# Optimization experiments

Measured on AMD Instinct MI355X. Metric: run time of the kernel, lower is better.

The kernel has to match this reference:

```python
import jax, jax.numpy as jnp
import numpy as np

B, T, C, H = 2, 2048, 1024, 16
D = C // H  # head dim = 64


def setup_inputs() -> dict:
    key = jax.random.key(0)
    ks = jax.random.split(key, 3)
    x = jax.random.normal(ks[0], (B, T, C), dtype=jnp.float32)
    W_attn = jax.random.normal(ks[1], (C, 3 * C), dtype=jnp.float32) * (1.0 / np.sqrt(C))
    b_attn = jnp.zeros((3 * C,), dtype=jnp.float32)
    W_proj = jax.random.normal(ks[2], (C, C), dtype=jnp.float32) * (1.0 / np.sqrt(C))
    b_proj = jnp.zeros((C,), dtype=jnp.float32)
    return {"x": x, "W_attn": W_attn, "b_attn": b_attn, "W_proj": W_proj, "b_proj": b_proj}


def reference(x, W_attn, b_attn, W_proj, b_proj):
    Bb, Tt, Cc = x.shape
    qkv = x @ W_attn + b_attn                       # [B,T,3C]
    q, k, v = jnp.split(qkv, 3, axis=-1)            # each [B,T,C]
    q = q.reshape(Bb, Tt, H, D).transpose(0, 2, 1, 3)  # [B,H,T,D]
    k = k.reshape(Bb, Tt, H, D).transpose(0, 2, 1, 3)
    v = v.reshape(Bb, Tt, H, D).transpose(0, 2, 1, 3)
    # NOTE: original scales by 1/sqrt(n_embd), not 1/sqrt(head_dim)
    scale = 1.0 / np.sqrt(Cc)
    wei = jnp.einsum('bhqd,bhkd->bhqk', q, k) * scale  # [B,H,T,T]
    causal = jnp.tril(jnp.ones((Tt, Tt), dtype=bool))
    wei = jnp.where(causal, wei, -jnp.inf)
    wei = jax.nn.softmax(wei, axis=-1)
    out = jnp.einsum('bhqk,bhkd->bhqd', wei, v)        # [B,H,T,D]
    out = out.transpose(0, 2, 1, 3).reshape(Bb, Tt, Cc)
    return out @ W_proj + b_proj
```

## Files before the change

kernel.cpp:

```cpp
#include <hip/hip_runtime.h>


typedef short bfrag __attribute__((ext_vector_type(8)));
typedef float facc  __attribute__((ext_vector_type(4)));
typedef float f16v  __attribute__((ext_vector_type(16)));
typedef float f4v   __attribute__((ext_vector_type(4)));
typedef unsigned int u32x2 __attribute__((ext_vector_type(2)));
typedef unsigned int u32x4v __attribute__((ext_vector_type(4)));
typedef unsigned short u16;

#define MFMA16(a, b, c) __builtin_amdgcn_mfma_f32_16x16x32_bf16((a), (b), (c), 0, 0, 0)
#define MFMA32(a, b, c) __builtin_amdgcn_mfma_f32_32x32x16_bf16((a), (b), (c), 0, 0, 0)

__device__ __forceinline__ u16 f2bf(float f) {
  union { float f; unsigned u; } v; v.f = f;
  unsigned r = v.u + 0x7fffu + ((v.u >> 16) & 1u);
  return (u16)(r >> 16);
}

__device__ __forceinline__ unsigned cvtpk(float lo, float hi) {
  unsigned r;
  asm("v_cvt_pk_bf16_f32 %0, %1, %2" : "=v"(r) : "v"(lo), "v"(hi));
  return r;
}

__device__ __forceinline__ void async_lds16(const void* g, void* l) {
  __builtin_amdgcn_global_load_lds(
      (const __attribute__((address_space(1))) unsigned char*)g,
      (__attribute__((address_space(3))) unsigned char*)l, 16, 0, 0);
}


__global__ void cast_bf16_kernel(const float* __restrict__ s, u16* __restrict__ d, int n) {
  int i = (blockIdx.x * blockDim.x + threadIdx.x) * 4;
  if (i >= n) return;
  f4v v = *reinterpret_cast<const f4v*>(s + i);
  u32x2 w;
  w[0] = (unsigned)f2bf(v[0]) | ((unsigned)f2bf(v[1]) << 16);
  w[1] = (unsigned)f2bf(v[2]) | ((unsigned)f2bf(v[3]) << 16);
  *reinterpret_cast<u32x2*>(d + i) = w;
}

__global__ void transpose_cast_kernel(const float* __restrict__ src, u16* __restrict__ dst,
                                      int K, int N) {
  __shared__ float tile[32][33];
  int tx = threadIdx.x, ty = threadIdx.y;
  int n0 = blockIdx.x * 32, k0 = blockIdx.y * 32;
  for (int j = ty; j < 32; j += 8)
    tile[j][tx] = src[(size_t)(k0 + j) * N + (n0 + tx)];
  __syncthreads();
  for (int j = ty; j < 32; j += 8)
    dst[(size_t)(n0 + j) * K + (k0 + tx)] = f2bf(tile[tx][j]);
}


template <int EPI>
__global__ __launch_bounds__(256) void gemm_kernel(
    const u16* __restrict__ A, const u16* __restrict__ Bt,
    const float* __restrict__ bias, float* __restrict__ outf,
    u16* __restrict__ qb, u16* __restrict__ kb, u16* __restrict__ vb, int NX) {
  constexpr int KD = 1024, NK = KD / 32;
  __shared__ u16 As[2][128 * 32];
  __shared__ u16 Bs[2][128 * 32];
  const int t = threadIdx.x;
  const int l = t & 63, w = t >> 6;
  const int wm = w >> 1, wn = w & 1;
  const int lg = l >> 4, lc = l & 15;
  const int nwg = gridDim.x;
  const int u = blockIdx.x;
  const int swz = (u & 7) * (nwg >> 3) + (u >> 3);
  const int m0 = (swz / NX) * 128, n0 = (swz % NX) * 128;
  facc acc[4][4] = {};
  const int srow = t >> 2, scol = (t & 3) * 8;
  const u16* ga = A + (size_t)(m0 + srow) * KD + scol;
  const u16* gb = Bt + (size_t)(n0 + srow) * KD + scol;

#define GSTAGE(bi, kt_)                                                          \
  {                                                                              \
    async_lds16(ga + (kt_) * 32, As[bi] + t * 8);                                \
    async_lds16(ga + 64 * KD + (kt_) * 32, As[bi] + 2048 + t * 8);               \
    async_lds16(gb + (kt_) * 32, Bs[bi] + t * 8);                                \
    async_lds16(gb + 64 * KD + (kt_) * 32, Bs[bi] + 2048 + t * 8);               \
  }

  GSTAGE(0, 0);
  __syncthreads();
  for (int kt = 0; kt < NK; ++kt) {
    const int buf = kt & 1;
    if (kt + 1 < NK) GSTAGE(buf ^ 1, kt + 1);
    bfrag a[4], b[4];
#pragma unroll
    for (int mi = 0; mi < 4; ++mi)
      a[mi] = *reinterpret_cast<const bfrag*>(As[buf] + (wm * 64 + mi * 16 + lc) * 32 + lg * 8);
#pragma unroll
    for (int ni = 0; ni < 4; ++ni)
      b[ni] = *reinterpret_cast<const bfrag*>(Bs[buf] + (wn * 64 + ni * 16 + lc) * 32 + lg * 8);
#pragma unroll
    for (int mi = 0; mi < 4; ++mi)
#pragma unroll
      for (int ni = 0; ni < 4; ++ni)
        acc[mi][ni] = MFMA16(a[mi], b[ni], acc[mi][ni]);
    __syncthreads();
  }
#undef GSTAGE
#pragma unroll
  for (int mi = 0; mi < 4; ++mi) {
#pragma unroll
    for (int ni = 0; ni < 4; ++ni) {
#pragma unroll
      for (int r = 0; r < 4; ++r) {
        int gm = m0 + wm * 64 + mi * 16 + lg * 4 + r;
        int gn = n0 + wn * 64 + ni * 16 + lc;
        float val = acc[mi][ni][r] + bias[gn];
        if constexpr (EPI == 0) {
          int sec = gn >> 10, ci = gn & 1023;
          int h = ci >> 6, d = ci & 63;
          int b_ = gm >> 11, tq = gm & 2047;
          int bh = b_ * 16 + h;
          if (sec == 0) {
            qb[((size_t)bh * 2048 + tq) * 64 + d] = f2bf(val * 0.045084439f);
          } else if (sec == 1) {
            kb[((size_t)bh * 2048 + tq) * 64 + d] = f2bf(val);
          } else {
            vb[((size_t)bh * 64 + d) * 2048 + tq] = f2bf(val);
          }
        } else {
          outf[(size_t)gm * 1024 + gn] = val;
        }
      }
    }
  }
}


__global__ __launch_bounds__(256, 2) void attn_kernel(
    const u16* __restrict__ Qb, const u16* __restrict__ Kb,
    const u16* __restrict__ Vtb, u16* __restrict__ attn) {
  constexpr int T = 2048;
  __shared__ u16 Ks[2][2][64 * 64];
  const int t = threadIdx.x;
  const int l = t & 63, w = t >> 6;
  const int wq = w >> 1, ws = w & 1;
  const int c = l & 31, h = l >> 5;
  const int b = blockIdx.x;
  const int bh = b & 31;
  const int qblk = 31 - (b >> 5);
  const int ntile = qblk + 1;
  const int nrounds = (ntile + 1) >> 1;
  const int q0 = qblk * 64 + wq * 32;
  const size_t base = (size_t)bh * T * 64;
  const u16* Qp = Qb + base;
  const u16* Kp = Kb + base;
  const u16* Vp = Vtb + base;

  bfrag qf[4];
#pragma unroll
  for (int dt = 0; dt < 4; ++dt)
    qf[dt] = *reinterpret_cast<const bfrag*>(Qp + (size_t)(q0 + c) * 64 + dt * 16 + 8 * h);

  f16v o[2] = {};
  f16v s[2];
  float m_ = -1e30f, l_ = 0.f;

  const int srow0 = wq * 8 + (l >> 3);
  const int sw8   = ((l & 7) ^ ((l >> 3) & 7)) * 8;
  const int ldso  = wq * 512 + l * 8;

#define STAGE_K(p, tile_)                                                        \
  {                                                                              \
    _Pragma("unroll")                                                            \
    for (int j = 0; j < 4; ++j)                                                  \
      async_lds16(Kp + (size_t)(64 * (tile_) + srow0 + 16 * j) * 64 + sw8,       \
                  &Ks[p][ws][ldso + 1024 * j]);                                  \
  }
#define LOADV(vf, kvb_)                                                          \
  {                                                                              \
    _Pragma("unroll")                                                            \
    for (int nt = 0; nt < 2; ++nt)                                               \
      _Pragma("unroll")                                                          \
      for (int k2 = 0; k2 < 4; ++k2)                                             \
        vf[nt * 4 + k2] = *reinterpret_cast<const bfrag*>(                       \
            Vp + (size_t)(32 * nt + c) * T + (kvb_) + 16 * k2 + 8 * h);          \
  }

  auto qk = [&](const u16* ks) {
    const f16v z = {};
    s[0] = z; s[1] = z;
    __builtin_amdgcn_s_setprio(1);
#pragma unroll
    for (int kt = 0; kt < 2; ++kt)
#pragma unroll
      for (int dt = 0; dt < 4; ++dt) {
        const bfrag a = *reinterpret_cast<const bfrag*>(
            ks + (32 * kt + c) * 64 + (((2 * dt + h) ^ (c & 7)) * 8));
        s[kt] = MFMA32(a, qf[dt], s[kt]);
      }
    __builtin_amdgcn_s_setprio(0);
  };

  auto pv = [&](const bfrag pa[4], const bfrag vf[8]) {
    __builtin_amdgcn_s_setprio(1);
#pragma unroll
    for (int nt = 0; nt < 2; ++nt)
#pragma unroll
      for (int k2 = 0; k2 < 4; ++k2)
        o[nt] = MFMA32(pa[k2], vf[nt * 4 + k2], o[nt]);
    __builtin_amdgcn_s_setprio(0);
  };

  auto softmax_pa = [&](int it, bfrag pa[4]) {
    if (it == ntile - 1) {
      const int kvb = 64 * it;
      const int qq = q0 + c;
#pragma unroll
      for (int kt = 0; kt < 2; ++kt)
#pragma unroll
        for (int r = 0; r < 16; ++r) {
          const int kk = kvb + 32 * kt + (r & 3) + 8 * (r >> 2) + 4 * h;
          if (kk > qq) s[kt][r] = -1e30f;
        }
    }
    float pms[4] = {-1e30f, -1e30f, -1e30f, -1e30f};
#pragma unroll
    for (int kt = 0; kt < 2; ++kt)
#pragma unroll
      for (int r = 0; r < 16; ++r) pms[r & 3] = fmaxf(pms[r & 3], s[kt][r]);
    float pm = fmaxf(fmaxf(pms[0], pms[1]), fmaxf(pms[2], pms[3]));
    pm = fmaxf(pm, __shfl_xor(pm, 32));
    if (!__all(pm <= m_ + 8.0f)) {
      const float mn = fmaxf(m_, pm);
      const float al = exp2f(m_ - mn);
      l_ *= al;
#pragma unroll
      for (int r = 0; r < 16; ++r) {
        const float ar = __shfl(al, (r & 3) + 8 * (r >> 2) + 4 * h);
        o[0][r] *= ar;
        o[1][r] *= ar;
      }
      m_ = mn;
    }
    float ps[4] = {0.f, 0.f, 0.f, 0.f};
#pragma unroll
    for (int kt = 0; kt < 2; ++kt)
#pragma unroll
      for (int r = 0; r < 16; ++r) {
        const float e = exp2f(s[kt][r] - m_);
        s[kt][r] = e;
        ps[r & 3] += e;
      }
    float pss = (ps[0] + ps[1]) + (ps[2] + ps[3]);
    pss += __shfl_xor(pss, 32);
    l_ += pss;
#pragma unroll
    for (int kt = 0; kt < 2; ++kt)
#pragma unroll
      for (int sub = 0; sub < 2; ++sub) {
        const int bs = 8 * sub;
        unsigned x1 = cvtpk(s[kt][bs + 0], s[kt][bs + 1]);
        unsigned y1 = cvtpk(s[kt][bs + 4], s[kt][bs + 5]);
        asm volatile("v_permlane32_swap_b32 %0, %1" : "+v"(x1), "+v"(y1));
        unsigned x2 = cvtpk(s[kt][bs + 2], s[kt][bs + 3]);
        unsigned y2 = cvtpk(s[kt][bs + 6], s[kt][bs + 7]);
        asm volatile("v_permlane32_swap_b32 %0, %1" : "+v"(x2), "+v"(y2));
        union { u32x4v wv; bfrag f; } u;
        u.wv[0] = x1; u.wv[1] = x2; u.wv[2] = y1; u.wv[3] = y2;
        pa[2 * kt + sub] = u.f;
      }
  };

  bfrag vfA[8], vfB[8], pa[4];
  if (ws < ntile) { STAGE_K(0, ws); LOADV(vfA, 64 * ws); }
  __syncthreads();
  for (int r = 0; r < nrounds; ++r) {
    const int p = r & 1;
    const int it = 2 * r + ws;
    const int itn = it + 2;
    if (itn < ntile) {
      STAGE_K(p ^ 1, itn);
      if (p) { LOADV(vfA, 64 * itn); } else { LOADV(vfB, 64 * itn); }
    }
    if (it < ntile) {
      qk(&Ks[p][ws][0]);
      softmax_pa(it, pa);
      pv(pa, p ? vfB : vfA);
    }
    __syncthreads();
  }

  float* Fo = (float*)&Ks[0][0][0];
  float* Fm = Fo + 2 * 64 * 33;
  float* Fl = Fm + 64;
  if (ws == 1) {
#pragma unroll
    for (int nt = 0; nt < 2; ++nt)
#pragma unroll
      for (int r = 0; r < 16; ++r) {
        const int row = (r & 3) + 8 * (r >> 2) + 4 * h;
        Fo[(wq * 64 + nt * 32 + c) * 33 + row] = o[nt][r];
      }
    if (h == 0) { Fm[wq * 32 + c] = m_; Fl[wq * 32 + c] = l_; }
  }
  __syncthreads();
  if (ws == 0) {
    const float m1v = Fm[wq * 32 + c], l1v = Fl[wq * 32 + c];
    const float mm = fmaxf(m_, m1v);
    const float a0 = exp2f(m_ - mm), a1 = exp2f(m1v - mm);
    const float linv = 1.0f / (a0 * l_ + a1 * l1v);
    const int b_ = bh >> 4, hd = bh & 15;
#pragma unroll
    for (int r = 0; r < 16; ++r) {
      const int row = (r & 3) + 8 * (r >> 2) + 4 * h;
      const float a0r = __shfl(a0, row);
      const float a1r = __shfl(a1, row);
      const float lr = __shfl(linv, row);
      const int tq = q0 + row;
#pragma unroll
      for (int nt = 0; nt < 2; ++nt) {
        const float o1 = Fo[(wq * 64 + nt * 32 + c) * 33 + row];
        attn[((size_t)(b_ * T + tq)) * 1024 + hd * 64 + 32 * nt + c] =
            f2bf((a0r * o[nt][r] + a1r * o1) * lr);
      }
    }
  }
#undef STAGE_K
#undef LOADV
}


extern "C" void kernel_launch(void* const* d_in, const int* in_sizes, int n_in,
                              void* d_out, int out_size, void* d_ws, size_t ws_size,
                              hipStream_t stream) {
  const float* x      = (const float*)d_in[0];
  const float* W_attn = (const float*)d_in[1];
  const float* b_attn = (const float*)d_in[2];
  const float* W_proj = (const float*)d_in[3];
  const float* b_proj = (const float*)d_in[4];
  float* out = (float*)d_out;
  char* ws = (char*)d_ws;
  u16* xb   = (u16*)(ws);
  u16* Wat  = (u16*)(ws + (8u  << 20));
  u16* Wpt  = (u16*)(ws + (14u << 20));
  u16* Qb   = (u16*)(ws + (16u << 20));
  u16* Kb   = (u16*)(ws + (24u << 20));
  u16* Vtb  = (u16*)(ws + (32u << 20));
  u16* attn = (u16*)(ws + (40u << 20));

  cast_bf16_kernel<<<4096, 256, 0, stream>>>(x, xb, 4096 * 1024);
  transpose_cast_kernel<<<dim3(96, 32), dim3(32, 8), 0, stream>>>(W_attn, Wat, 1024, 3072);
  transpose_cast_kernel<<<dim3(32, 32), dim3(32, 8), 0, stream>>>(W_proj, Wpt, 1024, 1024);
  gemm_kernel<0><<<768, 256, 0, stream>>>(xb, Wat, b_attn, nullptr, Qb, Kb, Vtb, 24);
  attn_kernel<<<1024, 256, 0, stream>>>(Qb, Kb, Vtb, attn);
  gemm_kernel<1><<<256, 256, 0, stream>>>(attn, Wpt, b_proj, out, nullptr, nullptr, nullptr, 8);
}
```

Measured before the change: 148.7 us.

## Drop GEMM double buffering and XCD swizzle, reorder attention query blocks

The GEMM goes back to a single LDS buffer, loading each K-slice between two barriers so the global-to-LDS copy no longer overlaps with MFMA work. It also drops the XCD-aware block swizzle in favour of a plain 2D grid. Separately, the attention kernel's query-block order changes from strictly longest-first to an interleaved long/short sequence across groups of 8, aiming at better load balance. The GEMM changes remove overlap and L2 locality, and the new attention order may leave long blocks in the tail.

After: 151.9 us. 2.2% more time.

```diff
diff --git a/kernel.cpp b/kernel.cpp
--- a/kernel.cpp
+++ b/kernel.cpp
@@ -58,51 +58,41 @@
 __global__ __launch_bounds__(256) void gemm_kernel(
     const u16* __restrict__ A, const u16* __restrict__ Bt,
     const float* __restrict__ bias, float* __restrict__ outf,
-    u16* __restrict__ qb, u16* __restrict__ kb, u16* __restrict__ vb, int NX) {
-  constexpr int KD = 1024, NK = KD / 32;
-  __shared__ u16 As[2][128 * 32];
-  __shared__ u16 Bs[2][128 * 32];
+    u16* __restrict__ qb, u16* __restrict__ kb, u16* __restrict__ vb) {
+  constexpr int KD = 1024;
+  __shared__ u16 As[128 * 32];
+  __shared__ u16 Bs[128 * 32];
   const int t = threadIdx.x;
   const int l = t & 63, w = t >> 6;
   const int wm = w >> 1, wn = w & 1;
   const int lg = l >> 4, lc = l & 15;
-  const int nwg = gridDim.x;
-  const int u = blockIdx.x;
-  const int swz = (u & 7) * (nwg >> 3) + (u >> 3);
-  const int m0 = (swz / NX) * 128, n0 = (swz % NX) * 128;
+  const int m0 = blockIdx.y * 128, n0 = blockIdx.x * 128;
   facc acc[4][4] = {};
   const int srow = t >> 2, scol = (t & 3) * 8;
   const u16* ga = A + (size_t)(m0 + srow) * KD + scol;
   const u16* gb = Bt + (size_t)(n0 + srow) * KD + scol;
-
-#define GSTAGE(bi, kt_)                                                          \
-  {                                                                              \
-    async_lds16(ga + (kt_) * 32, As[bi] + t * 8);                                \
-    async_lds16(ga + 64 * KD + (kt_) * 32, As[bi] + 2048 + t * 8);               \
-    async_lds16(gb + (kt_) * 32, Bs[bi] + t * 8);                                \
-    async_lds16(gb + 64 * KD + (kt_) * 32, Bs[bi] + 2048 + t * 8);               \
-  }
-
-  GSTAGE(0, 0);
-  __syncthreads();
-  for (int kt = 0; kt < NK; ++kt) {
-    const int buf = kt & 1;
-    if (kt + 1 < NK) GSTAGE(buf ^ 1, kt + 1);
+  u16* la0 = As + t * 8;  u16* la1 = As + 2048 + t * 8;
+  u16* lb0 = Bs + t * 8;  u16* lb1 = Bs + 2048 + t * 8;
+  for (int kt = 0; kt < KD / 32; ++kt) {
+    __syncthreads();
+    async_lds16(ga + kt * 32, la0);
+    async_lds16(ga + 64 * KD + kt * 32, la1);
+    async_lds16(gb + kt * 32, lb0);
+    async_lds16(gb + 64 * KD + kt * 32, lb1);
+    __syncthreads();
     bfrag a[4], b[4];
 #pragma unroll
     for (int mi = 0; mi < 4; ++mi)
-      a[mi] = *reinterpret_cast<const bfrag*>(As[buf] + (wm * 64 + mi * 16 + lc) * 32 + lg * 8);
+      a[mi] = *reinterpret_cast<const bfrag*>(As + (wm * 64 + mi * 16 + lc) * 32 + lg * 8);
 #pragma unroll
     for (int ni = 0; ni < 4; ++ni)
-      b[ni] = *reinterpret_cast<const bfrag*>(Bs[buf] + (wn * 64 + ni * 16 + lc) * 32 + lg * 8);
+      b[ni] = *reinterpret_cast<const bfrag*>(Bs + (wn * 64 + ni * 16 + lc) * 32 + lg * 8);
 #pragma unroll
     for (int mi = 0; mi < 4; ++mi)
 #pragma unroll
       for (int ni = 0; ni < 4; ++ni)
         acc[mi][ni] = MFMA16(a[mi], b[ni], acc[mi][ni]);
-    __syncthreads();
-  }
-#undef GSTAGE
+  }
 #pragma unroll
   for (int mi = 0; mi < 4; ++mi) {
 #pragma unroll
@@ -144,7 +134,8 @@
   const int c = l & 31, h = l >> 5;
   const int b = blockIdx.x;
   const int bh = b & 31;
-  const int qblk = 31 - (b >> 5);
+  const int g = b >> 5;
+  const int qblk = (g < 8) ? 31 - g : (g < 16) ? g - 8 : (g < 24) ? 39 - g : g - 16;
   const int ntile = qblk + 1;
   const int nrounds = (ntile + 1) >> 1;
   const int q0 = qblk * 64 + wq * 32;
@@ -348,7 +339,7 @@
   cast_bf16_kernel<<<4096, 256, 0, stream>>>(x, xb, 4096 * 1024);
   transpose_cast_kernel<<<dim3(96, 32), dim3(32, 8), 0, stream>>>(W_attn, Wat, 1024, 3072);
   transpose_cast_kernel<<<dim3(32, 32), dim3(32, 8), 0, stream>>>(W_proj, Wpt, 1024, 1024);
-  gemm_kernel<0><<<768, 256, 0, stream>>>(xb, Wat, b_attn, nullptr, Qb, Kb, Vtb, 24);
+  gemm_kernel<0><<<dim3(24, 32), 256, 0, stream>>>(xb, Wat, b_attn, nullptr, Qb, Kb, Vtb);
   attn_kernel<<<1024, 256, 0, stream>>>(Qb, Kb, Vtb, attn);
-  gemm_kernel<1><<<256, 256, 0, stream>>>(attn, Wpt, b_proj, out, nullptr, nullptr, nullptr, 8);
-}
+  gemm_kernel<1><<<dim3(8, 32), 256, 0, stream>>>(attn, Wpt, b_proj, out, nullptr, nullptr, nullptr);
+}
```
